# Performance work log

Hardware: AMD Instinct MI355X
Metric: run time of the kernel (lower is better)

## Reference

```python
import jax, jax.numpy as jnp
import numpy as np

N_NODES = 50000
N_EDGES = 800000
N_GRAPHS = 128
IN_DIM, HID_DIM, OUT_DIM = 128, 96, 10


def setup_inputs() -> dict:
    key = jax.random.key(0)
    ks = jax.random.split(key, 9)
    x = jax.random.normal(ks[0], (N_NODES, IN_DIM), dtype=jnp.float32)
    edge_index = jax.random.randint(ks[1], (2, N_EDGES), 0, N_NODES, dtype=jnp.int32)
    batch = jnp.sort(jax.random.randint(ks[2], (N_NODES,), 0, N_GRAPHS, dtype=jnp.int32))
    s1 = 1.0 / np.sqrt(IN_DIM)
    s2 = 1.0 / np.sqrt(HID_DIM)
    W1 = jax.random.uniform(ks[3], (IN_DIM, HID_DIM), jnp.float32, -s1, s1)
    b1 = jnp.zeros((HID_DIM,), jnp.float32)
    W2 = jax.random.uniform(ks[4], (HID_DIM, HID_DIM), jnp.float32, -s2, s2)
    b2 = jnp.zeros((HID_DIM,), jnp.float32)
    Wf = jax.random.uniform(ks[5], (OUT_DIM, HID_DIM), jnp.float32, -s2, s2)
    bf = jax.random.uniform(ks[6], (OUT_DIM,), jnp.float32, -s2, s2)
    return {"x": x, "edge_index": edge_index, "batch": batch,
            "W1": W1, "b1": b1, "W2": W2, "b2": b2, "Wf": Wf, "bf": bf}


def reference(x, edge_index, batch, W1, b1, W2, b2, Wf, bf):
    n = x.shape[0]
    row, col = edge_index[0], edge_index[1]
    # GCN symmetric normalization with self-loops: deg = 1 + in-degree
    deg = jax.ops.segment_sum(jnp.ones_like(col, dtype=x.dtype), col, num_segments=n) + 1.0
    dinv = deg ** -0.5  # [N]
    norm = dinv[row] * dinv[col]  # [E]

    def gcn_conv(h, W, b):
        h = h @ W  # [N, F_out]
        # edge messages: norm_e * h[src] scattered to dst; self-loops handled analytically
        agg = jax.ops.segment_sum(norm[:, None] * h[row], col, num_segments=n)
        agg = agg + (dinv * dinv)[:, None] * h
        return agg + b

    h = jax.nn.relu(gcn_conv(x, W1, b1))
    h = gcn_conv(h, W2, b2)

    # global mean pool over graphs
    counts = jax.ops.segment_sum(jnp.ones((n,), x.dtype), batch, num_segments=N_GRAPHS)
    pooled = jax.ops.segment_sum(h, batch, num_segments=N_GRAPHS)
    pooled = pooled / jnp.maximum(counts, 1.0)[:, None]

    logits = pooled @ Wf.T + bf
    return jax.nn.log_softmax(logits, axis=1)
```

## Files before the change

### kernel.cpp

```cpp
#include <hip/hip_runtime.h>
#include <hip/hip_bf16.h>

#define N_GRAPHS 128
#define HID 96
#define OUT_DIM 10
#define CAP 64

typedef __attribute__((ext_vector_type(8))) short short8;
typedef __attribute__((ext_vector_type(4))) float f32x4;
typedef __attribute__((ext_vector_type(2))) float f32x2;

__device__ inline unsigned short f2bf(float f) {
    union { float f; unsigned u; } x;
    x.f = f;
    unsigned r = x.u + 0x7FFFu + ((x.u >> 16) & 1u);
    return (unsigned short)(r >> 16);
}

__device__ inline unsigned char f2fp8(float v) {
    int p = __builtin_amdgcn_cvt_pk_fp8_f32(v, v, 0, false);
    return (unsigned char)(p & 0xff);
}

__device__ inline void unpack16_fp8(uint4 v, float* o) {
    f32x2 a0 = __builtin_amdgcn_cvt_pk_f32_fp8((int)v.x, false);
    f32x2 a1 = __builtin_amdgcn_cvt_pk_f32_fp8((int)v.x, true);
    f32x2 b0 = __builtin_amdgcn_cvt_pk_f32_fp8((int)v.y, false);
    f32x2 b1 = __builtin_amdgcn_cvt_pk_f32_fp8((int)v.y, true);
    f32x2 c0 = __builtin_amdgcn_cvt_pk_f32_fp8((int)v.z, false);
    f32x2 c1 = __builtin_amdgcn_cvt_pk_f32_fp8((int)v.z, true);
    f32x2 d0 = __builtin_amdgcn_cvt_pk_f32_fp8((int)v.w, false);
    f32x2 d1 = __builtin_amdgcn_cvt_pk_f32_fp8((int)v.w, true);
    o[0] = a0.x;  o[1] = a0.y;  o[2] = a1.x;  o[3] = a1.y;
    o[4] = b0.x;  o[5] = b0.y;  o[6] = b1.x;  o[7] = b1.y;
    o[8] = c0.x;  o[9] = c0.y;  o[10] = c1.x; o[11] = c1.y;
    o[12] = d0.x; o[13] = d0.y; o[14] = d1.x; o[15] = d1.y;
}

__global__ __launch_bounds__(256) void fill_kernel(const int* __restrict__ rowi,
                                                   const int* __restrict__ coli,
                                                   int* __restrict__ cnt,
                                                   unsigned short* __restrict__ srcs,
                                                   int E, int N) {
    const int part = blockIdx.x & 7;
    const int chunk = blockIdx.x >> 3;
    const int base = chunk * 2048;
    const int plo = (int)(((long long)N * part) >> 3);
    const int phi = (int)(((long long)N * (part + 1)) >> 3);
#pragma unroll
    for (int it = 0; it < 8; ++it) {
        int e = base + it * 256 + threadIdx.x;
        if (e < E) {
            int c = coli[e];
            if (c >= plo && c < phi) {
                int pos = atomicAdd(&cnt[c], 1);
                if (pos < CAP) srcs[(size_t)c * CAP + pos] = (unsigned short)rowi[e];
            }
        }
    }
}

__global__ __launch_bounds__(256) void gemm1_mfma(const float* __restrict__ X,
                                                  const float* __restrict__ W,
                                                  const int* __restrict__ cnt,
                                                  unsigned char* __restrict__ Tp, int N) {
    constexpr int K = 128;
    constexpr int P = K + 8;
    constexpr int KT = K / 32;
    __shared__ __align__(16) unsigned short Wt[96 * P];
    const int tid = threadIdx.x;
    const int row0 = blockIdx.x * 64;

    for (int idx = tid; idx < K * 96; idx += 256) {
        int k = idx / 96, n = idx - k * 96;
        Wt[n * P + k] = f2bf(W[idx]);
    }
    __syncthreads();

    const int wv = tid >> 6;
    const int lane = tid & 63;
    const int m = lane & 15;
    const int quad = lane >> 4;
    const int row = row0 + wv * 16 + m;

    short8 afrag[KT];
    if (row < N) {
        const float* Xr = X + (size_t)row * K;
#pragma unroll
        for (int t = 0; t < KT; ++t) {
            float4 a0 = *(const float4*)(Xr + t * 32 + quad * 8);
            float4 a1 = *(const float4*)(Xr + t * 32 + quad * 8 + 4);
            short8 a;
            a[0] = (short)f2bf(a0.x); a[1] = (short)f2bf(a0.y);
            a[2] = (short)f2bf(a0.z); a[3] = (short)f2bf(a0.w);
            a[4] = (short)f2bf(a1.x); a[5] = (short)f2bf(a1.y);
            a[6] = (short)f2bf(a1.z); a[7] = (short)f2bf(a1.w);
            afrag[t] = a;
        }
    } else {
#pragma unroll
        for (int t = 0; t < KT; ++t) afrag[t] = short8{0, 0, 0, 0, 0, 0, 0, 0};
    }

    f32x4 acc[6];
#pragma unroll
    for (int nt = 0; nt < 6; ++nt) acc[nt] = f32x4{0.f, 0.f, 0.f, 0.f};
#pragma unroll
    for (int t = 0; t < KT; ++t) {
#pragma unroll
        for (int nt = 0; nt < 6; ++nt) {
            short8 bfrag = *(const short8*)&Wt[(nt * 16 + m) * P + t * 32 + quad * 8];
            acc[nt] = __builtin_amdgcn_mfma_f32_16x16x32_bf16(afrag[t], bfrag, acc[nt], 0, 0, 0);
        }
    }
#pragma unroll
    for (int r = 0; r < 4; ++r) {
        int orow = row0 + wv * 16 + quad * 4 + r;
        if (orow < N) {
            float d = rsqrtf(1.0f + (float)cnt[orow]);
#pragma unroll
            for (int nt = 0; nt < 6; ++nt)
                Tp[(size_t)orow * 96 + nt * 16 + m] = f2fp8(d * acc[nt][r]);
        }
    }
}

__global__ __launch_bounds__(256) void gather1_gemm2(const unsigned char* __restrict__ Tp1,
                                                     const unsigned short* __restrict__ srcs,
                                                     const int* __restrict__ cnt,
                                                     const float* __restrict__ b1,
                                                     const float* __restrict__ W2,
                                                     unsigned char* __restrict__ Tp2, int N) {
    constexpr int PH = 104;
    constexpr int PW = 104;
    __shared__ __align__(16) unsigned short Hs[128 * PH];
    __shared__ __align__(16) unsigned short Wt[96 * PW];
    const int tid = threadIdx.x;
    const int node0 = blockIdx.x * 128;

    for (int idx = tid; idx < 96 * 96; idx += 256) {
        int k = idx / 96, n = idx - k * 96;
        Wt[n * PW + k] = f2bf(W2[idx]);
    }

    const uint4* Trow = (const uint4*)Tp1;
#pragma unroll
    for (int it = 0; it < 3; ++it) {
        int idx = it * 256 + tid;
        int n = idx / 6, j = idx - n * 6;
        int i = node0 + n;
        if (i < N) {
            float acc[16], tmp[16];
            unpack16_fp8(Trow[(size_t)i * 6 + j], acc);
            int ci = cnt[i];
            int e = min(ci, CAP);
            const unsigned short* sp = srcs + (size_t)i * CAP;
            int k = 0;
            for (; k + 4 <= e; k += 4) {
                ushort4 s4 = *(const ushort4*)(sp + k);
                uint4 v0 = Trow[(size_t)s4.x * 6 + j];
                uint4 v1 = Trow[(size_t)s4.y * 6 + j];
                uint4 v2 = Trow[(size_t)s4.z * 6 + j];
                uint4 v3 = Trow[(size_t)s4.w * 6 + j];
                unpack16_fp8(v0, tmp);
#pragma unroll
                for (int l = 0; l < 16; ++l) acc[l] += tmp[l];
                unpack16_fp8(v1, tmp);
#pragma unroll
                for (int l = 0; l < 16; ++l) acc[l] += tmp[l];
                unpack16_fp8(v2, tmp);
#pragma unroll
                for (int l = 0; l < 16; ++l) acc[l] += tmp[l];
                unpack16_fp8(v3, tmp);
#pragma unroll
                for (int l = 0; l < 16; ++l) acc[l] += tmp[l];
            }
            for (; k < e; ++k) {
                unpack16_fp8(Trow[(size_t)sp[k] * 6 + j], tmp);
#pragma unroll
                for (int l = 0; l < 16; ++l) acc[l] += tmp[l];
            }
            float di = rsqrtf(1.0f + (float)ci);
#pragma unroll
            for (int l = 0; l < 16; ++l) {
                float v = fmaxf(di * acc[l] + b1[j * 16 + l], 0.0f);
                Hs[n * PH + j * 16 + l] = f2bf(v);
            }
        } else {
#pragma unroll
            for (int l = 0; l < 16; ++l) Hs[n * PH + j * 16 + l] = 0;
        }
    }
    __syncthreads();

    const int wv = tid >> 6;
    const int lane = tid & 63;
    const int m = lane & 15;
    const int quad = lane >> 4;
#pragma unroll
    for (int half = 0; half < 2; ++half) {
        const int rt = wv + half * 4;
        const int lrow = rt * 16 + m;
        short8 afrag[3];
#pragma unroll
        for (int t = 0; t < 3; ++t)
            afrag[t] = *(const short8*)&Hs[lrow * PH + t * 32 + quad * 8];
        f32x4 acc[6];
#pragma unroll
        for (int nt = 0; nt < 6; ++nt) acc[nt] = f32x4{0.f, 0.f, 0.f, 0.f};
#pragma unroll
        for (int t = 0; t < 3; ++t) {
#pragma unroll
            for (int nt = 0; nt < 6; ++nt) {
                short8 bfrag = *(const short8*)&Wt[(nt * 16 + m) * PW + t * 32 + quad * 8];
                acc[nt] = __builtin_amdgcn_mfma_f32_16x16x32_bf16(afrag[t], bfrag, acc[nt], 0, 0, 0);
            }
        }
#pragma unroll
        for (int r = 0; r < 4; ++r) {
            int orow = node0 + rt * 16 + quad * 4 + r;
            if (orow < N) {
                float d = rsqrtf(1.0f + (float)cnt[orow]);
#pragma unroll
                for (int nt = 0; nt < 6; ++nt)
                    Tp2[(size_t)orow * 96 + nt * 16 + m] = f2fp8(d * acc[nt][r]);
            }
        }
    }
}

__global__ __launch_bounds__(192) void gather2_pool(const unsigned char* __restrict__ Tp,
                                                    const unsigned short* __restrict__ srcs,
                                                    const int* __restrict__ cnt,
                                                    const int* __restrict__ batch,
                                                    float* __restrict__ pooled, int N) {
    __shared__ float hl[32 * 96];
    __shared__ int g_l[32];
    const int tid = threadIdx.x;
    const int n = tid / 6;
    const int j = tid - n * 6;
    const int i = blockIdx.x * 32 + n;
    if (tid < 32) {
        int ii = blockIdx.x * 32 + tid;
        g_l[tid] = (ii < N) ? batch[ii] : -1;
    }

    float acc[16];
#pragma unroll
    for (int l = 0; l < 16; ++l) acc[l] = 0.0f;
    float di = 0.0f;
    if (i < N) {
        const uint4* Trow = (const uint4*)Tp;
        float tmp[16];
        unpack16_fp8(Trow[(size_t)i * 6 + j], acc);
        int ci = cnt[i];
        di = rsqrtf(1.0f + (float)ci);
        int e = min(ci, CAP);
        const unsigned short* sp = srcs + (size_t)i * CAP;
        int k = 0;
        for (; k + 4 <= e; k += 4) {
            ushort4 s4 = *(const ushort4*)(sp + k);
            uint4 v0 = Trow[(size_t)s4.x * 6 + j];
            uint4 v1 = Trow[(size_t)s4.y * 6 + j];
            uint4 v2 = Trow[(size_t)s4.z * 6 + j];
            uint4 v3 = Trow[(size_t)s4.w * 6 + j];
            unpack16_fp8(v0, tmp);
#pragma unroll
            for (int l = 0; l < 16; ++l) acc[l] += tmp[l];
            unpack16_fp8(v1, tmp);
#pragma unroll
            for (int l = 0; l < 16; ++l) acc[l] += tmp[l];
            unpack16_fp8(v2, tmp);
#pragma unroll
            for (int l = 0; l < 16; ++l) acc[l] += tmp[l];
            unpack16_fp8(v3, tmp);
#pragma unroll
            for (int l = 0; l < 16; ++l) acc[l] += tmp[l];
        }
        for (; k < e; ++k) {
            unpack16_fp8(Trow[(size_t)sp[k] * 6 + j], tmp);
#pragma unroll
            for (int l = 0; l < 16; ++l) acc[l] += tmp[l];
        }
    }
#pragma unroll
    for (int l = 0; l < 16; ++l) hl[n * 96 + j * 16 + l] = di * acc[l];
    __syncthreads();

    if (tid < 96) {
        int f = tid;
        float s = 0.0f;
        int gcur = -2;
        for (int nn = 0; nn < 32; ++nn) {
            int g = g_l[nn];
            if (g < 0) continue;
            if (g != gcur) {
                if (gcur >= 0) atomicAdd(&pooled[gcur * 96 + f], s);
                gcur = g;
                s = 0.0f;
            }
            s += hl[nn * 96 + f];
        }
        if (gcur >= 0) atomicAdd(&pooled[gcur * 96 + f], s);
    }
}

__device__ inline int lower_bound_dev(const int* __restrict__ a, int n, int val) {
    int lo = 0, hi = n;
    while (lo < hi) {
        int m = (lo + hi) >> 1;
        if (a[m] < val) lo = m + 1; else hi = m;
    }
    return lo;
}

__global__ void head_kernel(const float* __restrict__ pooled, const int* __restrict__ batch,
                            const float* __restrict__ b2, const float* __restrict__ Wf,
                            const float* __restrict__ bfv, float* __restrict__ out, int N) {
    __shared__ float wfs[OUT_DIM * HID];
    __shared__ float b2s[HID];
    __shared__ float bfs[OUT_DIM];
    int t = threadIdx.x;
    for (int idx = t; idx < OUT_DIM * HID; idx += 128) wfs[idx] = Wf[idx];
    if (t < HID) b2s[t] = b2[t];
    if (t < OUT_DIM) bfs[t] = bfv[t];
    __syncthreads();
    int g = t;
    if (g >= N_GRAPHS) return;
    int lo = lower_bound_dev(batch, N, g);
    int hi = lower_bound_dev(batch, N, g + 1);
    int c = hi - lo;
    float inv = (c > 0) ? 1.0f / (float)c : 0.0f;
    float hasb = (c > 0) ? 1.0f : 0.0f;
    float logits[OUT_DIM];
#pragma unroll
    for (int o = 0; o < OUT_DIM; ++o) {
        float s = 0.0f;
        for (int cc = 0; cc < HID; ++cc)
            s += (pooled[g * HID + cc] * inv + hasb * b2s[cc]) * wfs[o * HID + cc];
        logits[o] = s + bfs[o];
    }
    float m = logits[0];
#pragma unroll
    for (int o = 1; o < OUT_DIM; ++o) m = fmaxf(m, logits[o]);
    float se = 0.0f;
#pragma unroll
    for (int o = 0; o < OUT_DIM; ++o) se += expf(logits[o] - m);
    float lse = m + logf(se);
#pragma unroll
    for (int o = 0; o < OUT_DIM; ++o) out[g * OUT_DIM + o] = logits[o] - lse;
}

extern "C" void kernel_launch(void* const* d_in, const int* in_sizes, int n_in,
                              void* d_out, int out_size, void* d_ws, size_t ws_size,
                              hipStream_t stream) {
    const float* x     = (const float*)d_in[0];
    const int*   ei    = (const int*)d_in[1];
    const int*   batch = (const int*)d_in[2];
    const float* W1    = (const float*)d_in[3];
    const float* b1    = (const float*)d_in[4];
    const float* W2    = (const float*)d_in[5];
    const float* b2    = (const float*)d_in[6];
    const float* Wf    = (const float*)d_in[7];
    const float* bf    = (const float*)d_in[8];

    const int N = in_sizes[0] / 128;
    const int E = in_sizes[1] / 2;
    const int* rowi = ei;
    const int* coli = ei + E;

    size_t off = 0;
    auto alloc = [&](size_t bytes) {
        void* p = (char*)d_ws + off;
        off += (bytes + 255) & ~(size_t)255;
        return p;
    };
    int*            cnt    = (int*)alloc((size_t)N * 4);
    float*          pooled = (float*)alloc((size_t)N_GRAPHS * HID * 4);
    size_t zero_bytes = off;
    unsigned short* srcs   = (unsigned short*)alloc((size_t)N * CAP * 2);
    unsigned char*  Tp1    = (unsigned char*)alloc((size_t)N * HID);
    unsigned char*  Tp2    = (unsigned char*)alloc((size_t)N * HID);

    hipMemsetAsync(d_ws, 0, zero_bytes, stream);

    const int nchunk = (E + 2047) / 2048;
    fill_kernel<<<nchunk * 8, 256, 0, stream>>>(rowi, coli, cnt, srcs, E, N);

    gemm1_mfma<<<(N + 63) / 64, 256, 0, stream>>>(x, W1, cnt, Tp1, N);

    gather1_gemm2<<<(N + 127) / 128, 256, 0, stream>>>(Tp1, srcs, cnt, b1, W2, Tp2, N);

    gather2_pool<<<(N + 31) / 32, 192, 0, stream>>>(Tp2, srcs, cnt, batch, pooled, N);

    head_kernel<<<1, 128, 0, stream>>>(pooled, batch, b2, Wf, bf, (float*)d_out, N);
}
```

Measured before the change: 215.2 us.

## Pad fp8 feature rows to 128 bytes and unroll gather by eight

```diff
diff --git a/kernel.cpp b/kernel.cpp
--- a/kernel.cpp
+++ b/kernel.cpp
@@ -5,8 +5,10 @@
 #define HID 96
 #define OUT_DIM 10
 #define CAP 64
+#define TROW 128
 
 typedef __attribute__((ext_vector_type(8))) short short8;
+typedef __attribute__((ext_vector_type(8))) unsigned short ushort8v;
 typedef __attribute__((ext_vector_type(4))) float f32x4;
 typedef __attribute__((ext_vector_type(2))) float f32x2;
 
@@ -120,7 +122,7 @@
             float d = rsqrtf(1.0f + (float)cnt[orow]);
 #pragma unroll
             for (int nt = 0; nt < 6; ++nt)
-                Tp[(size_t)orow * 96 + nt * 16 + m] = f2fp8(d * acc[nt][r]);
+                Tp[(size_t)orow * TROW + nt * 16 + m] = f2fp8(d * acc[nt][r]);
         }
     }
 }
@@ -151,17 +153,52 @@
         int i = node0 + n;
         if (i < N) {
             float acc[16], tmp[16];
-            unpack16_fp8(Trow[(size_t)i * 6 + j], acc);
+            unpack16_fp8(Trow[((size_t)i << 3) + j], acc);
             int ci = cnt[i];
             int e = min(ci, CAP);
             const unsigned short* sp = srcs + (size_t)i * CAP;
             int k = 0;
+            for (; k + 8 <= e; k += 8) {
+                ushort8v s8 = *(const ushort8v*)(sp + k);
+                uint4 v0 = Trow[((size_t)s8[0] << 3) + j];
+                uint4 v1 = Trow[((size_t)s8[1] << 3) + j];
+                uint4 v2 = Trow[((size_t)s8[2] << 3) + j];
+                uint4 v3 = Trow[((size_t)s8[3] << 3) + j];
+                uint4 v4 = Trow[((size_t)s8[4] << 3) + j];
+                uint4 v5 = Trow[((size_t)s8[5] << 3) + j];
+                uint4 v6 = Trow[((size_t)s8[6] << 3) + j];
+                uint4 v7 = Trow[((size_t)s8[7] << 3) + j];
+                unpack16_fp8(v0, tmp);
+#pragma unroll
+                for (int l = 0; l < 16; ++l) acc[l] += tmp[l];
+                unpack16_fp8(v1, tmp);
+#pragma unroll
+                for (int l = 0; l < 16; ++l) acc[l] += tmp[l];
+                unpack16_fp8(v2, tmp);
+#pragma unroll
+                for (int l = 0; l < 16; ++l) acc[l] += tmp[l];
+                unpack16_fp8(v3, tmp);
+#pragma unroll
+                for (int l = 0; l < 16; ++l) acc[l] += tmp[l];
+                unpack16_fp8(v4, tmp);
+#pragma unroll
+                for (int l = 0; l < 16; ++l) acc[l] += tmp[l];
+                unpack16_fp8(v5, tmp);
+#pragma unroll
+                for (int l = 0; l < 16; ++l) acc[l] += tmp[l];
+                unpack16_fp8(v6, tmp);
+#pragma unroll
+                for (int l = 0; l < 16; ++l) acc[l] += tmp[l];
+                unpack16_fp8(v7, tmp);
+#pragma unroll
+                for (int l = 0; l < 16; ++l) acc[l] += tmp[l];
+            }
             for (; k + 4 <= e; k += 4) {
                 ushort4 s4 = *(const ushort4*)(sp + k);
-                uint4 v0 = Trow[(size_t)s4.x * 6 + j];
-                uint4 v1 = Trow[(size_t)s4.y * 6 + j];
-                uint4 v2 = Trow[(size_t)s4.z * 6 + j];
-                uint4 v3 = Trow[(size_t)s4.w * 6 + j];
+                uint4 v0 = Trow[((size_t)s4.x << 3) + j];
+                uint4 v1 = Trow[((size_t)s4.y << 3) + j];
+                uint4 v2 = Trow[((size_t)s4.z << 3) + j];
+                uint4 v3 = Trow[((size_t)s4.w << 3) + j];
                 unpack16_fp8(v0, tmp);
 #pragma unroll
                 for (int l = 0; l < 16; ++l) acc[l] += tmp[l];
@@ -176,7 +213,7 @@
                 for (int l = 0; l < 16; ++l) acc[l] += tmp[l];
             }
             for (; k < e; ++k) {
-                unpack16_fp8(Trow[(size_t)sp[k] * 6 + j], tmp);
+                unpack16_fp8(Trow[((size_t)sp[k] << 3) + j], tmp);
 #pragma unroll
                 for (int l = 0; l < 16; ++l) acc[l] += tmp[l];
             }
@@ -223,7 +260,7 @@
                 float d = rsqrtf(1.0f + (float)cnt[orow]);
 #pragma unroll
                 for (int nt = 0; nt < 6; ++nt)
-                    Tp2[(size_t)orow * 96 + nt * 16 + m] = f2fp8(d * acc[nt][r]);
+                    Tp2[(size_t)orow * TROW + nt * 16 + m] = f2fp8(d * acc[nt][r]);
             }
         }
     }
@@ -252,18 +289,53 @@
     if (i < N) {
         const uint4* Trow = (const uint4*)Tp;
         float tmp[16];
-        unpack16_fp8(Trow[(size_t)i * 6 + j], acc);
+        unpack16_fp8(Trow[((size_t)i << 3) + j], acc);
         int ci = cnt[i];
         di = rsqrtf(1.0f + (float)ci);
         int e = min(ci, CAP);
         const unsigned short* sp = srcs + (size_t)i * CAP;
         int k = 0;
+        for (; k + 8 <= e; k += 8) {
+            ushort8v s8 = *(const ushort8v*)(sp + k);
+            uint4 v0 = Trow[((size_t)s8[0] << 3) + j];
+            uint4 v1 = Trow[((size_t)s8[1] << 3) + j];
+            uint4 v2 = Trow[((size_t)s8[2] << 3) + j];
+            uint4 v3 = Trow[((size_t)s8[3] << 3) + j];
+            uint4 v4 = Trow[((size_t)s8[4] << 3) + j];
+            uint4 v5 = Trow[((size_t)s8[5] << 3) + j];
+            uint4 v6 = Trow[((size_t)s8[6] << 3) + j];
+            uint4 v7 = Trow[((size_t)s8[7] << 3) + j];
+            unpack16_fp8(v0, tmp);
+#pragma unroll
+            for (int l = 0; l < 16; ++l) acc[l] += tmp[l];
+            unpack16_fp8(v1, tmp);
+#pragma unroll
+            for (int l = 0; l < 16; ++l) acc[l] += tmp[l];
+            unpack16_fp8(v2, tmp);
+#pragma unroll
+            for (int l = 0; l < 16; ++l) acc[l] += tmp[l];
+            unpack16_fp8(v3, tmp);
+#pragma unroll
+            for (int l = 0; l < 16; ++l) acc[l] += tmp[l];
+            unpack16_fp8(v4, tmp);
+#pragma unroll
+            for (int l = 0; l < 16; ++l) acc[l] += tmp[l];
+            unpack16_fp8(v5, tmp);
+#pragma unroll
+            for (int l = 0; l < 16; ++l) acc[l] += tmp[l];
+            unpack16_fp8(v6, tmp);
+#pragma unroll
+            for (int l = 0; l < 16; ++l) acc[l] += tmp[l];
+            unpack16_fp8(v7, tmp);
+#pragma unroll
+            for (int l = 0; l < 16; ++l) acc[l] += tmp[l];
+        }
         for (; k + 4 <= e; k += 4) {
             ushort4 s4 = *(const ushort4*)(sp + k);
-            uint4 v0 = Trow[(size_t)s4.x * 6 + j];
-            uint4 v1 = Trow[(size_t)s4.y * 6 + j];
-            uint4 v2 = Trow[(size_t)s4.z * 6 + j];
-            uint4 v3 = Trow[(size_t)s4.w * 6 + j];
+            uint4 v0 = Trow[((size_t)s4.x << 3) + j];
+            uint4 v1 = Trow[((size_t)s4.y << 3) + j];
+            uint4 v2 = Trow[((size_t)s4.z << 3) + j];
+            uint4 v3 = Trow[((size_t)s4.w << 3) + j];
             unpack16_fp8(v0, tmp);
 #pragma unroll
             for (int l = 0; l < 16; ++l) acc[l] += tmp[l];
@@ -278,7 +350,7 @@
             for (int l = 0; l < 16; ++l) acc[l] += tmp[l];
         }
         for (; k < e; ++k) {
-            unpack16_fp8(Trow[(size_t)sp[k] * 6 + j], tmp);
+            unpack16_fp8(Trow[((size_t)sp[k] << 3) + j], tmp);
 #pragma unroll
             for (int l = 0; l < 16; ++l) acc[l] += tmp[l];
         }
@@ -379,8 +451,8 @@
     float*          pooled = (float*)alloc((size_t)N_GRAPHS * HID * 4);
     size_t zero_bytes = off;
     unsigned short* srcs   = (unsigned short*)alloc((size_t)N * CAP * 2);
-    unsigned char*  Tp1    = (unsigned char*)alloc((size_t)N * HID);
-    unsigned char*  Tp2    = (unsigned char*)alloc((size_t)N * HID);
+    unsigned char*  Tp1    = (unsigned char*)alloc((size_t)N * TROW);
+    unsigned char*  Tp2    = (unsigned char*)alloc((size_t)N * TROW);
 
     hipMemsetAsync(d_ws, 0, zero_bytes, stream);
 
```

Measured after the change: 213.6 us. About the same (-0.8%).
